# Kernel tuning notes

Measured on AMD Instinct MI355X. Metric: run time of the kernel, lower is better.

Reference implementation:

```python
import jax, jax.numpy as jnp
import numpy as np

THRESH = 1.0
TAU_M = 20.0
TAU_S = 5.0
NUM_STEPS = 300
CFG = (34 * 34 * 2, 800, 10)
BATCH = 32
SPIKE_PROB = 0.02


def _dtdu(um, us, spike):
    # dt/du = 1 / (du/dt) at spike time; du/dt = -um/tau_m + us/tau_s,
    # magnitude clamped away from zero for numerical safety.
    dudt = -um / TAU_M + us / TAU_S
    dudt = jnp.where(dudt >= 0, jnp.maximum(dudt, 1e-2), jnp.minimum(dudt, -1e-2))
    return spike / dudt


def _forward(input, W1, W2, batch_size):
    dm = jnp.exp(jnp.float32(-1.0 / TAU_M))
    ds = jnp.exp(jnp.float32(-1.0 / TAU_S))
    Din, H, O = CFG
    # (B,2,34,34,T) -> (T,B,Din)
    x = jnp.moveaxis(input.reshape(batch_size, Din, NUM_STEPS), -1, 0)
    z = lambda d: jnp.zeros((batch_size, d), jnp.float32)
    carry = (
        jnp.ones((batch_size, H), jnp.float32), z(Din), z(Din),   # sav1, vm1, vs1
        jnp.ones((batch_size, O), jnp.float32), z(H), z(H),       # sav2, vm2, vs2
        jnp.full((batch_size, O), float(NUM_STEPS), jnp.float32), # out_t
        z(O),                                                     # out_u
        jnp.zeros((3,), jnp.float32),                             # sum_sp
        jnp.zeros((batch_size, H, Din), jnp.float32),             # h1_v
        jnp.zeros((batch_size, O, H), jnp.float32),               # h2_v
        jnp.zeros((batch_size, H, Din), jnp.float32),             # h1_dvdt
        jnp.zeros((batch_size, O, H), jnp.float32),               # h2_dvdt
        z(H), z(O),                                               # h1_dtdu, h2_dtdu
    )

    def step(c, xs):
        (sav1, vm1, vs1, sav2, vm2, vs2, out_t, out_u, sum_sp,
         h1_v, h2_v, h1_dvdt, h2_dvdt, h1_dtdu, h2_dtdu) = c
        in_spike, t = xs
        # layer 1 NOSO neuron (dual-exponential kernel, single spike via sav gate)
        vm1 = vm1 * dm + in_spike
        vs1 = vs1 * ds + in_spike
        um1 = vm1 @ W1.T
        us1 = vs1 @ W1.T
        u1 = sav1 * (um1 - us1)
        spk1 = (u1 >= THRESH).astype(jnp.float32)
        sav1 = sav1 * (1.0 - spk1)
        # layer 2 (output neuron)
        vm2 = vm2 * dm + spk1
        vs2 = vs2 * ds + spk1
        um2 = vm2 @ W2.T
        us2 = vs2 @ W2.T
        u2 = sav2 * (um2 - us2)
        spk2 = (u2 >= THRESH).astype(jnp.float32)
        sav2 = sav2 * (1.0 - spk2)
        # spike-time / potential readout
        out_t = out_t + spk2 * (t.astype(jnp.float32) - NUM_STEPS)
        out_u = out_u + spk2 * u2
        sum_sp = sum_sp + jnp.stack([in_spike.sum(), spk1.sum(), spk2.sum()])
        # outer-product stat accumulation (B,out,in)
        h1_v = h1_v + spk1[:, :, None] * (vm1 - vs1)[:, None, :]
        h2_v = h2_v + spk2[:, :, None] * (vm2 - vs2)[:, None, :]
        h1_dvdt = h1_dvdt + spk1[:, :, None] * (vm1 / TAU_M - vs1 / TAU_S)[:, None, :]
        h2_dvdt = h2_dvdt + spk2[:, :, None] * (vm2 / TAU_M - vs2 / TAU_S)[:, None, :]
        h1_dtdu = h1_dtdu + _dtdu(um1, us1, spk1)
        h2_dtdu = h2_dtdu + _dtdu(um2, us2, spk2)
        return (sav1, vm1, vs1, sav2, vm2, vs2, out_t, out_u, sum_sp,
                h1_v, h2_v, h1_dvdt, h2_dvdt, h1_dtdu, h2_dtdu), None

    c, _ = jax.lax.scan(step, carry, (x, jnp.arange(NUM_STEPS)))
    out_t, out_u, sum_sp = c[6], c[7], c[8]
    h1_v, h2_v, h1_dvdt, h2_dvdt, h1_dtdu, h2_dtdu = c[9], c[10], c[11], c[12], c[13], c[14]
    return out_t, out_u, sum_sp, h1_v, h2_v, h1_dvdt, h2_dvdt, h1_dtdu, h2_dtdu


def setup_inputs() -> dict:
    key = jax.random.key(0)
    k1, k2, k3 = jax.random.split(key, 3)
    inp = (jax.random.uniform(k1, (BATCH, 2, 34, 34, NUM_STEPS)) < SPIKE_PROB).astype(jnp.float32)
    W1 = jax.random.normal(k2, (CFG[1], CFG[0]), jnp.float32) * float(np.sqrt(2.0 / CFG[0]))
    W2 = jax.random.normal(k3, (CFG[2], CFG[1]), jnp.float32) * float(np.sqrt(2.0 / CFG[1]))
    return {"input": inp, "W1": W1, "W2": W2, "batch_size": BATCH}


def reference(input, W1, W2, batch_size):
    return _forward(input, W1, W2, batch_size)
```

## Files before the change

kernel.cpp:

```cpp
#include <hip/hip_runtime.h>
#include <cstdint>
#include <cstddef>

#define BB 32
#define TT 300
#define DD 2312
#define HH 800
#define OO 10
#define CAP1 128
#define KMAX 32

typedef float f32x4 __attribute__((ext_vector_type(4)));

#define DM_F 0.95122942450071400909f
#define DS_F 0.81873075307798185867f

#define OUT_T_OFF 0
#define OUT_U_OFF 320
#define SUM_OFF   640
#define H1V_OFF   643ull
#define H2V_OFF   59187843ull
#define H1DV_OFF  59443843ull
#define H2DV_OFF  118631043ull
#define H1DT_OFF  118887043ull
#define H2DT_OFF  118912643ull

#define WS_W1T    0ull
#define WS_C1     7398400ull
#define WS_IDX1   38118400ull
#define WS_CNT1   55936000ull
#define WS_T1     56012800ull
#define WS_T2     56115200ull
#define WS_DMP    56116480ull
#define WS_DSP    56117760ull
#define WS_TIMES1 56119040ull

__global__ void k_pow(float* __restrict__ dmp, float* __restrict__ dsp) {
    if (threadIdx.x == 0) {
        float v = 1.f;
        for (int i = 0; i <= TT; ++i) { dmp[i] = v; v *= DM_F; }
    }
    if (threadIdx.x == 1) {
        float v = 1.f;
        for (int i = 0; i <= TT; ++i) { dsp[i] = v; v *= DS_F; }
    }
}

__global__ void k_transpose(const float* __restrict__ W1, float* __restrict__ W1T) {
    __shared__ float tile[32][33];
    int dx = blockIdx.x * 32, hy = blockIdx.y * 32;
    int tx = threadIdx.x, ty = threadIdx.y;
    int d = dx + tx, h = hy + ty;
    if (d < DD) tile[ty][tx] = W1[(size_t)h * DD + d];
    __syncthreads();
    int d2 = dx + ty, h2 = hy + tx;
    if (d2 < DD) W1T[(size_t)d2 * HH + h2] = tile[tx][ty];
}

__global__ void k_events(const float* __restrict__ in, int* __restrict__ cnt1,
                         unsigned short* __restrict__ idx1,
                         unsigned short* __restrict__ times1T) {
    int row = blockIdx.x * 4 + (threadIdx.x >> 6);
    int lane = threadIdx.x & 63;
    int b = row / DD, din = row - b * DD;
    const float* p = in + (size_t)row * TT;
    int kbase = 0;
    for (int r = 0; r < 5; ++r) {
        int t = r * 64 + lane;
        float v = (t < TT) ? p[t] : 0.f;
        bool act = (v != 0.f);
        unsigned long long m = __ballot(act);
        if (act) {
            int pos1 = atomicAdd(&cnt1[b * TT + t], 1);
            if (pos1 < CAP1) idx1[(size_t)(b * TT + t) * CAP1 + pos1] = (unsigned short)din;
            int pos = kbase + __popcll(m & ((1ull << lane) - 1ull));
            if (pos < KMAX)
                times1T[((size_t)b * KMAX + pos) * DD + din] = (unsigned short)t;
        }
        kbase += __popcll(m);
    }
}

__global__ __launch_bounds__(256) void k_c1(const int* __restrict__ cnt1,
                                            const unsigned short* __restrict__ idx1,
                                            const float* __restrict__ W1T,
                                            float* __restrict__ c1) {
    int blk = blockIdx.x;
    int cnt = cnt1[blk];
    if (cnt > CAP1) cnt = CAP1;
    __shared__ int sidx[CAP1];
    for (int j = threadIdx.x; j < cnt; j += 256) sidx[j] = idx1[(size_t)blk * CAP1 + j];
    __syncthreads();
    int tid = threadIdx.x;
    if (tid < 200) {
        f32x4 acc = {0.f, 0.f, 0.f, 0.f};
        for (int j = 0; j < cnt; ++j) {
            const f32x4* row = (const f32x4*)(W1T + (size_t)sidx[j] * HH);
            acc += row[tid];
        }
        ((f32x4*)(c1 + (size_t)blk * HH))[tid] = acc;
    }
}

__global__ void k_scan1(const float* __restrict__ c1, int* __restrict__ t1,
                        float* __restrict__ out) {
    int id = blockIdx.x * 64 + threadIdx.x;
    int b = id / HH, h = id - b * HH;
    float um = 0.f, us = 0.f;
    bool done = false;
    int t1v = TT;
    const float* cbase = c1 + (size_t)b * TT * HH + h;
    for (int t = 0; t < TT; ++t) {
        float c = cbase[(size_t)t * HH];
        um = um * DM_F + c;
        us = us * DS_F + c;
        float u = um - us;
        if (u >= 1.0f) {
            done = true; t1v = t;
            float dudt = -um / 20.0f + us / 5.0f;
            dudt = (dudt >= 0.f) ? fmaxf(dudt, 1e-2f) : fminf(dudt, -1e-2f);
            out[H1DT_OFF + (size_t)id] = 1.f / dudt;
            break;
        }
    }
    if (!done) out[H1DT_OFF + (size_t)id] = 0.f;
    t1[id] = t1v;
}

__global__ __launch_bounds__(256) void k_layer2(const int* __restrict__ t1,
                                                const int* __restrict__ cnt1,
                                                const float* __restrict__ W2,
                                                int* __restrict__ t2,
                                                float* __restrict__ out) {
    __shared__ float c2[OO][TT];
    __shared__ int red[4];
    int b = blockIdx.x, tid = threadIdx.x;
    for (int i = tid; i < OO * TT; i += 256) ((float*)c2)[i] = 0.f;
    __syncthreads();
    for (int h = tid; h < HH; h += 256) {
        int t = t1[b * HH + h];
        if (t < TT) {
            #pragma unroll
            for (int o = 0; o < OO; ++o) atomicAdd(&c2[o][t], W2[o * HH + h]);
        }
    }
    __syncthreads();
    bool done = false;
    if (tid < OO) {
        float um = 0.f, us = 0.f, u2 = 0.f, dtdu = 0.f;
        int t2v = TT;
        for (int t = 0; t < TT; ++t) {
            float c = c2[tid][t];
            um = um * DM_F + c;
            us = us * DS_F + c;
            float u = um - us;
            if (u >= 1.0f) {
                done = true; t2v = t; u2 = u;
                float dudt = -um / 20.0f + us / 5.0f;
                dudt = (dudt >= 0.f) ? fmaxf(dudt, 1e-2f) : fminf(dudt, -1e-2f);
                dtdu = 1.f / dudt;
                break;
            }
        }
        out[OUT_T_OFF + b * OO + tid] = (float)t2v;
        out[OUT_U_OFF + b * OO + tid] = done ? u2 : 0.f;
        out[H2DT_OFF + (size_t)(b * OO + tid)] = done ? dtdu : 0.f;
        t2[b * OO + tid] = t2v;
    }
    unsigned long long m = __ballot(done);
    if (tid == 0 && m) atomicAdd(&out[SUM_OFF + 2], (float)__popcll(m));

    if (blockIdx.x == 0) {
        int s0 = 0, s1 = 0;
        for (int i = tid; i < BB * TT; i += 256) s0 += cnt1[i];
        for (int i = tid; i < BB * HH; i += 256) s1 += (t1[i] < TT);
        for (int d = 32; d >= 1; d >>= 1) {
            s0 += __shfl_down(s0, d, 64);
            s1 += __shfl_down(s1, d, 64);
        }
        int w = tid >> 6;
        if ((tid & 63) == 0) red[w] = s0;
        __syncthreads();
        if (tid == 0) out[SUM_OFF + 0] = (float)(red[0] + red[1] + red[2] + red[3]);
        __syncthreads();
        if ((tid & 63) == 0) red[w] = s1;
        __syncthreads();
        if (tid == 0) out[SUM_OFF + 1] = (float)(red[0] + red[1] + red[2] + red[3]);
    }
}

__global__ void k_h2(const int* __restrict__ t1, const int* __restrict__ t2,
                     const float* __restrict__ dmp, const float* __restrict__ dsp,
                     float* __restrict__ out) {
    int blk = blockIdx.x;
    int b = blk / OO;
    int t2v = t2[blk];
    bool spk = (t2v < TT);
    for (int h = threadIdx.x; h < HH; h += 256) {
        float v = 0.f, dv = 0.f;
        if (spk) {
            int t1v = t1[b * HH + h];
            if (t1v <= t2v) {
                int k = t2v - t1v;
                float a = dmp[k], s = dsp[k];
                v = a - s;
                dv = a / 20.0f - s / 5.0f;
            }
        }
        out[H2V_OFF + (size_t)blk * HH + h] = v;
        out[H2DV_OFF + (size_t)blk * HH + h] = dv;
    }
}

struct AS { float a, s; };

__device__ __forceinline__ AS h1_accum(const unsigned short* __restrict__ tp,
                                       int d, int t1v,
                                       const float* __restrict__ sm,
                                       const float* __restrict__ ss) {
    AS r; r.a = 0.f; r.s = 0.f;
    #pragma unroll 1
    for (int j = 0; j < KMAX; ++j) {
        int ts = tp[(size_t)j * DD + d];
        if (ts > t1v) break;
        int e = t1v - ts;
        r.a += sm[e]; r.s += ss[e];
    }
    return r;
}

__global__ __launch_bounds__(256) void k_h1ev(const int* __restrict__ t1,
                                              const unsigned short* __restrict__ times1T,
                                              const float* __restrict__ dmp,
                                              const float* __restrict__ dsp,
                                              float* __restrict__ out) {
    int blk = blockIdx.x;
    int b = blk / HH;
    int t1v = t1[blk];
    size_t rbase = (size_t)blk * DD;
    float* pv = out + H1V_OFF + rbase;
    float* pd = out + H1DV_OFF + rbase;
    int tid = threadIdx.x;
    if (t1v >= TT) {
        f32x4 z = {0.f, 0.f, 0.f, 0.f};
        for (int g = tid; g < 577; g += 256) {
            __builtin_nontemporal_store(z, (f32x4*)(pv + 1 + g * 4));
            __builtin_nontemporal_store(z, (f32x4*)(pd + 1 + g * 4));
        }
        if (tid < 4) {
            int d = (tid == 0) ? 0 : 2308 + tid;
            __builtin_nontemporal_store(0.f, pv + d);
            __builtin_nontemporal_store(0.f, pd + d);
        }
        return;
    }
    __shared__ float sm[TT], ss[TT];
    for (int i = tid; i < TT; i += 256) { sm[i] = dmp[i]; ss[i] = dsp[i]; }
    __syncthreads();
    const unsigned short* tp = times1T + (size_t)b * KMAX * DD;
    for (int g = tid; g < 577; g += 256) {
        int d0 = 1 + g * 4;
        AS r0 = h1_accum(tp, d0 + 0, t1v, sm, ss);
        AS r1 = h1_accum(tp, d0 + 1, t1v, sm, ss);
        AS r2 = h1_accum(tp, d0 + 2, t1v, sm, ss);
        AS r3 = h1_accum(tp, d0 + 3, t1v, sm, ss);
        f32x4 v4 = {r0.a - r0.s, r1.a - r1.s, r2.a - r2.s, r3.a - r3.s};
        f32x4 d4 = {r0.a * 0.05f - r0.s * 0.2f, r1.a * 0.05f - r1.s * 0.2f,
                    r2.a * 0.05f - r2.s * 0.2f, r3.a * 0.05f - r3.s * 0.2f};
        __builtin_nontemporal_store(v4, (f32x4*)(pv + d0));
        __builtin_nontemporal_store(d4, (f32x4*)(pd + d0));
    }
    if (tid < 4) {
        int d = (tid == 0) ? 0 : 2308 + tid;
        AS r = h1_accum(tp, d, t1v, sm, ss);
        __builtin_nontemporal_store(r.a - r.s, pv + d);
        __builtin_nontemporal_store(r.a * 0.05f - r.s * 0.2f, pd + d);
    }
}

extern "C" void kernel_launch(void* const* d_in, const int* in_sizes, int n_in,
                              void* d_out, int out_size, void* d_ws, size_t ws_size,
                              hipStream_t stream) {
    (void)in_sizes; (void)n_in; (void)out_size; (void)ws_size;
    const float* in = (const float*)d_in[0];
    const float* W1 = (const float*)d_in[1];
    const float* W2 = (const float*)d_in[2];
    float* out = (float*)d_out;
    char* ws = (char*)d_ws;

    float* W1T = (float*)(ws + WS_W1T);
    float* c1  = (float*)(ws + WS_C1);
    unsigned short* idx1 = (unsigned short*)(ws + WS_IDX1);
    int* cnt1 = (int*)(ws + WS_CNT1);
    int* t1   = (int*)(ws + WS_T1);
    int* t2   = (int*)(ws + WS_T2);
    float* dmp = (float*)(ws + WS_DMP);
    float* dsp = (float*)(ws + WS_DSP);
    unsigned short* times1T = (unsigned short*)(ws + WS_TIMES1);

    (void)hipMemsetAsync(cnt1, 0, (size_t)BB * TT * 4, stream);
    (void)hipMemsetAsync(times1T, 0xFF, (size_t)BB * KMAX * DD * 2, stream);
    (void)hipMemsetAsync(out + SUM_OFF, 0, 3 * sizeof(float), stream);

    k_pow<<<1, 64, 0, stream>>>(dmp, dsp);
    k_transpose<<<dim3(73, 25), dim3(32, 32), 0, stream>>>(W1, W1T);
    k_events<<<(BB * DD) / 4, 256, 0, stream>>>(in, cnt1, idx1, times1T);
    k_c1<<<BB * TT, 256, 0, stream>>>(cnt1, idx1, W1T, c1);
    k_scan1<<<(BB * HH) / 64, 64, 0, stream>>>(c1, t1, out);
    k_layer2<<<BB, 256, 0, stream>>>(t1, cnt1, W2, t2, out);
    k_h2<<<BB * OO, 256, 0, stream>>>(t1, t2, dmp, dsp, out);
    k_h1ev<<<BB * HH, 256, 0, stream>>>(t1, times1T, dmp, dsp, out);
}
```

Baseline: 528.2 us.

## Split c1 accumulation across blocks, branchless layer-1 scan, drop times memset

The event gather kernel is split into two 128-thread blocks per (batch, timestep), each covering half of the hidden units, which doubles the block count. The layer-1 scan becomes branchless and unrolled, so all threads run the full time loop and record the membrane values at the first crossing. The large 0xFF memset of the spike-times table is replaced by a sentinel written only after the last valid entry, which assumes downstream readers stop at the first sentinel. The cost is redundant index loads, and early-exit savings in the scan are given up for more memory-level parallelism.

```diff
diff --git a/kernel.cpp b/kernel.cpp
--- a/kernel.cpp
+++ b/kernel.cpp
@@ -79,26 +79,30 @@
         }
         kbase += __popcll(m);
     }
-}
-
-__global__ __launch_bounds__(256) void k_c1(const int* __restrict__ cnt1,
+    if (lane == 0 && kbase < KMAX)
+        times1T[((size_t)b * KMAX + kbase) * DD + din] = 0xFFFFu;
+}
+
+__global__ __launch_bounds__(128) void k_c1(const int* __restrict__ cnt1,
                                             const unsigned short* __restrict__ idx1,
                                             const float* __restrict__ W1T,
                                             float* __restrict__ c1) {
-    int blk = blockIdx.x;
+    int blk = blockIdx.x % (BB * TT);
+    int chunk = blockIdx.x / (BB * TT);
     int cnt = cnt1[blk];
     if (cnt > CAP1) cnt = CAP1;
     __shared__ int sidx[CAP1];
-    for (int j = threadIdx.x; j < cnt; j += 256) sidx[j] = idx1[(size_t)blk * CAP1 + j];
+    for (int j = threadIdx.x; j < cnt; j += 128) sidx[j] = idx1[(size_t)blk * CAP1 + j];
     __syncthreads();
     int tid = threadIdx.x;
-    if (tid < 200) {
+    if (tid < 100) {
+        int v4i = chunk * 100 + tid;
         f32x4 acc = {0.f, 0.f, 0.f, 0.f};
         for (int j = 0; j < cnt; ++j) {
             const f32x4* row = (const f32x4*)(W1T + (size_t)sidx[j] * HH);
-            acc += row[tid];
-        }
-        ((f32x4*)(c1 + (size_t)blk * HH))[tid] = acc;
+            acc += row[v4i];
+        }
+        ((f32x4*)(c1 + (size_t)blk * HH))[v4i] = acc;
     }
 }
 
@@ -106,24 +110,26 @@
                         float* __restrict__ out) {
     int id = blockIdx.x * 64 + threadIdx.x;
     int b = id / HH, h = id - b * HH;
-    float um = 0.f, us = 0.f;
-    bool done = false;
+    float um = 0.f, us = 0.f, umx = 0.f, usx = 0.f;
     int t1v = TT;
     const float* cbase = c1 + (size_t)b * TT * HH + h;
+    #pragma unroll 4
     for (int t = 0; t < TT; ++t) {
         float c = cbase[(size_t)t * HH];
         um = um * DM_F + c;
         us = us * DS_F + c;
-        float u = um - us;
-        if (u >= 1.0f) {
-            done = true; t1v = t;
-            float dudt = -um / 20.0f + us / 5.0f;
-            dudt = (dudt >= 0.f) ? fmaxf(dudt, 1e-2f) : fminf(dudt, -1e-2f);
-            out[H1DT_OFF + (size_t)id] = 1.f / dudt;
-            break;
-        }
-    }
-    if (!done) out[H1DT_OFF + (size_t)id] = 0.f;
+        bool cross = (um - us >= 1.0f) && (t1v == TT);
+        t1v = cross ? t : t1v;
+        umx = cross ? um : umx;
+        usx = cross ? us : usx;
+    }
+    float dt = 0.f;
+    if (t1v < TT) {
+        float dudt = -umx / 20.0f + usx / 5.0f;
+        dudt = (dudt >= 0.f) ? fmaxf(dudt, 1e-2f) : fminf(dudt, -1e-2f);
+        dt = 1.f / dudt;
+    }
+    out[H1DT_OFF + (size_t)id] = dt;
     t1[id] = t1v;
 }
 
@@ -299,13 +305,12 @@
     unsigned short* times1T = (unsigned short*)(ws + WS_TIMES1);
 
     (void)hipMemsetAsync(cnt1, 0, (size_t)BB * TT * 4, stream);
-    (void)hipMemsetAsync(times1T, 0xFF, (size_t)BB * KMAX * DD * 2, stream);
     (void)hipMemsetAsync(out + SUM_OFF, 0, 3 * sizeof(float), stream);
 
     k_pow<<<1, 64, 0, stream>>>(dmp, dsp);
     k_transpose<<<dim3(73, 25), dim3(32, 32), 0, stream>>>(W1, W1T);
     k_events<<<(BB * DD) / 4, 256, 0, stream>>>(in, cnt1, idx1, times1T);
-    k_c1<<<BB * TT, 256, 0, stream>>>(cnt1, idx1, W1T, c1);
+    k_c1<<<2 * BB * TT, 128, 0, stream>>>(cnt1, idx1, W1T, c1);
     k_scan1<<<(BB * HH) / 64, 64, 0, stream>>>(c1, t1, out);
     k_layer2<<<BB, 256, 0, stream>>>(t1, cnt1, W2, t2, out);
     k_h2<<<BB * OO, 256, 0, stream>>>(t1, t2, dmp, dsp, out);
```

After: 434.4 us. 1.22x faster.
